# Kernel tuning notes

Measured on AMD Instinct MI355X. Metric: run time of the kernel, lower is better.

## Reference

```python
import jax, jax.numpy as jnp
import numpy as np

N_NODES = 100000
N_EDGES = 600000
D = 128


def gcn_conv(x, W, b, src, dst, n_nodes):
    """PyG-style GCNConv: add self-loops, symmetric deg^{-1/2} normalization."""
    xw = x @ W  # [N, out]
    # degree of destination nodes, counting the added self-loop
    deg = jnp.zeros((n_nodes,), xw.dtype).at[dst].add(1.0) + 1.0
    dinv = jax.lax.rsqrt(deg)
    coef = dinv[src] * dinv[dst]  # [E]
    agg = jnp.zeros_like(xw).at[dst].add(xw[src] * coef[:, None])
    agg = agg + xw * (dinv * dinv)[:, None]  # self-loop term
    return agg + b


def setup_inputs() -> dict:
    key = jax.random.key(0)
    k = jax.random.split(key, 9)
    s = 1.0 / np.sqrt(D)
    return {
        "x": jax.random.normal(k[0], (N_NODES, D), jnp.float32),
        "edge_index_pos": jax.random.randint(k[1], (2, N_EDGES), 0, N_NODES, jnp.int64),
        "edge_index_neg": jax.random.randint(k[2], (2, N_EDGES), 0, N_NODES, jnp.int64),
        "W1": jax.random.uniform(k[3], (D, D), jnp.float32, -s, s),
        "b1": jnp.zeros((D,), jnp.float32),
        "W2": jax.random.uniform(k[4], (D, D), jnp.float32, -s, s),
        "b2": jnp.zeros((D,), jnp.float32),
        "weight": jax.random.uniform(k[5], (2 * D, D), jnp.float32, -s, s),
        "bias": jnp.zeros((D,), jnp.float32),
    }


def reference(x, edge_index_pos, edge_index_neg, W1, b1, W2, b2, weight, bias):
    n = x.shape[0]
    h1 = gcn_conv(x, W1, b1, edge_index_pos[0], edge_index_pos[1], n)  # [N, D]
    h2 = gcn_conv(x, W2, b2, edge_index_neg[0], edge_index_neg[1], n)  # [N, D]
    h = jnp.concatenate([h1, h2], axis=-1)  # [N, 2D]
    return h @ weight + bias  # [N, D]
```

## Files before the change

kernel.cpp:

```cpp
#include <hip/hip_runtime.h>

#define N_NODES 100000
#define NT (2 * N_NODES)
#define D 128
#define N_EDGES 600000
#define ET (2 * N_EDGES)
#define CAP 32
#define XBLK 12500
#define EGRID ((ET + 255) / 256)
#define FROWS 256
#define FBLK ((N_NODES + FROWS - 1) / FROWS)
#define NBLK2 ((NT + 255) / 256)

typedef __attribute__((ext_vector_type(8))) short bf16x8;
typedef __attribute__((ext_vector_type(4))) float f32x4;

__device__ __forceinline__ unsigned short f2bf(float f) {
    union { float f; unsigned u; } v; v.f = f;
    unsigned r = (v.u + 0x7fff + ((v.u >> 16) & 1)) >> 16;
    return (unsigned short)r;
}
__device__ __forceinline__ float bf2f(unsigned short h) {
    union { unsigned u; float f; } v; v.u = ((unsigned)h) << 16;
    return v.f;
}

__device__ __forceinline__ long long load_idx(const void* e, long long i, int is32) {
    if (is32) return (long long)((const int*)e)[i];
    return ((const long long*)e)[i];
}

__device__ __forceinline__ int self_detect(const unsigned long long* __restrict__ e) {
    unsigned long long v = e[threadIdx.x & 63];
    unsigned long long m = __ballot(v > 0xFFFFFFFFull);
    return (m != 0ull) ? 1 : 0;
}

__global__ void prep_x2bf_degree(const float* __restrict__ W1, const float* __restrict__ W2,
                                 const float* __restrict__ weight,
                                 const float* __restrict__ b1, const float* __restrict__ b2,
                                 const float* __restrict__ bias,
                                 const float* __restrict__ x, unsigned short* __restrict__ xb,
                                 const void* __restrict__ ep, const void* __restrict__ en,
                                 unsigned short* __restrict__ Mt, float* __restrict__ bt,
                                 int* __restrict__ cnt) {
    const int b = blockIdx.x;
    if (b < 128) {
        int idx = b * 256 + threadIdx.x;
        int j = idx >> 8, k = idx & 255;
        float a = 0.f;
        if (k < D) {
            for (int d = 0; d < D; ++d) a += W1[k * D + d] * weight[d * D + j];
        } else {
            for (int d = 0; d < D; ++d) a += W2[(k - D) * D + d] * weight[(D + d) * D + j];
        }
        Mt[j * 256 + k] = f2bf(a);
    } else if (b == 128) {
        int t = threadIdx.x;
        if (t < D) {
            float a = bias[t];
            for (int k = 0; k < D; ++k)
                a += b1[k] * weight[k * D + t] + b2[k] * weight[(D + k) * D + t];
            bt[t] = a;
        }
    } else if (b < 129 + XBLK) {
        long long t = (long long)(b - 129) * 256 + threadIdx.x;
        float4 a = ((const float4*)x)[t];
        ((ushort4*)xb)[t] = make_ushort4(f2bf(a.x), f2bf(a.y), f2bf(a.z), f2bf(a.w));
    } else {
        int is32 = self_detect((const unsigned long long*)ep);
        int i = (b - 129 - XBLK) * 256 + threadIdx.x;
        if (i >= ET) return;
        int conv = (i >= N_EDGES);
        const void* e = conv ? en : ep;
        int j = conv ? i - N_EDGES : i;
        long long d = load_idx(e, (long long)N_EDGES + j, is32);
        atomicAdd(&cnt[conv * N_NODES + (int)d], 1);
    }
}

__global__ void make_dinv(const int* __restrict__ cnt, float* __restrict__ dinv,
                          unsigned char* __restrict__ degb) {
    int i = blockIdx.x * 256 + threadIdx.x;
    if (i < NT) {
        int v = cnt[i];
        dinv[i] = rsqrtf((float)v + 1.0f);
        degb[i] = (unsigned char)(v > 255 ? 255 : v);
    }
}

__global__ void ell_fill(const void* __restrict__ ep_, const void* __restrict__ en_,
                         const unsigned char* __restrict__ degb,
                         int* __restrict__ cnt, unsigned* __restrict__ ell) {
    int is32 = self_detect((const unsigned long long*)ep_);
    int i = blockIdx.x * blockDim.x + threadIdx.x;
    if (i >= ET) return;
    int conv = (i >= N_EDGES);
    const void* e = conv ? en_ : ep_;
    int j = conv ? i - N_EDGES : i;
    int si = (int)load_idx(e, j, is32);
    int di = (int)load_idx(e, (long long)N_EDGES + j, is32);
    int g = conv * N_NODES;
    int node = g + di;
    int slot = atomicSub(&cnt[node], 1) - 1;
    if (slot >= 0 && slot < CAP) {
        unsigned degS = degb[g + si];
        ell[(size_t)node * CAP + slot] = (unsigned)si | (degS << 20);
    }
}

__global__ __launch_bounds__(1024) void fused_gather_gemm(
    const unsigned char* __restrict__ degb, const unsigned* __restrict__ ell,
    const unsigned short* __restrict__ xb, const float* __restrict__ dinv,
    const unsigned short* __restrict__ Mt, const float* __restrict__ bt,
    float* __restrict__ out) {
    __shared__ unsigned short mlds[128][264];
    int t = threadIdx.x;
    for (int c = t; c < 4096; c += 1024) {
        int row = c >> 5;
        int kc = (c & 31) * 8;
        *(ulonglong2*)&mlds[row][kc] = *(const ulonglong2*)&Mt[row * 256 + kc];
    }
    __syncthreads();

    int wave = t >> 6, lane = t & 63;
    int rl = lane & 15, q = lane >> 4;
    int gr = blockIdx.x * FROWS + wave * 16 + rl;
    const bool valid = gr < N_NODES;

    bf16x8 af[8];
    #pragma unroll
    for (int conv = 0; conv < 2; ++conv) {
        float acc[4][8];
        if (valid) {
            int n = conv * N_NODES + gr;
            float dn = dinv[n];
            float f = dn * dn;
            const unsigned short* xr = xb + (size_t)gr * D + q * 8;
            #pragma unroll
            for (int m = 0; m < 4; ++m) {
                bf16x8 v = *(const bf16x8*)(xr + m * 32);
                #pragma unroll
                for (int j = 0; j < 8; ++j) acc[m][j] = bf2f((unsigned short)v[j]) * f;
            }
            int deg = degb[n];
            if (deg > CAP) deg = CAP;
            const unsigned* ep = ell + (size_t)n * CAP;
            int e = 0;
            for (; e + 1 < deg; e += 2) {
                unsigned c0 = ep[e], c1 = ep[e + 1];
                const unsigned short* p0 = xb + (size_t)(c0 & 0xFFFFF) * D + q * 8;
                const unsigned short* p1 = xb + (size_t)(c1 & 0xFFFFF) * D + q * 8;
                bf16x8 a0 = *(const bf16x8*)(p0);
                bf16x8 a1 = *(const bf16x8*)(p0 + 32);
                bf16x8 a2 = *(const bf16x8*)(p0 + 64);
                bf16x8 a3 = *(const bf16x8*)(p0 + 96);
                bf16x8 b0 = *(const bf16x8*)(p1);
                bf16x8 b1 = *(const bf16x8*)(p1 + 32);
                bf16x8 b2 = *(const bf16x8*)(p1 + 64);
                bf16x8 b3 = *(const bf16x8*)(p1 + 96);
                float coef0 = dn * rsqrtf((float)(c0 >> 20) + 1.0f);
                float coef1 = dn * rsqrtf((float)(c1 >> 20) + 1.0f);
                #pragma unroll
                for (int j = 0; j < 8; ++j) {
                    acc[0][j] += coef0 * bf2f((unsigned short)a0[j]);
                    acc[1][j] += coef0 * bf2f((unsigned short)a1[j]);
                    acc[2][j] += coef0 * bf2f((unsigned short)a2[j]);
                    acc[3][j] += coef0 * bf2f((unsigned short)a3[j]);
                }
                #pragma unroll
                for (int j = 0; j < 8; ++j) {
                    acc[0][j] += coef1 * bf2f((unsigned short)b0[j]);
                    acc[1][j] += coef1 * bf2f((unsigned short)b1[j]);
                    acc[2][j] += coef1 * bf2f((unsigned short)b2[j]);
                    acc[3][j] += coef1 * bf2f((unsigned short)b3[j]);
                }
            }
            if (e < deg) {
                unsigned c0 = ep[e];
                const unsigned short* p0 = xb + (size_t)(c0 & 0xFFFFF) * D + q * 8;
                bf16x8 a0 = *(const bf16x8*)(p0);
                bf16x8 a1 = *(const bf16x8*)(p0 + 32);
                bf16x8 a2 = *(const bf16x8*)(p0 + 64);
                bf16x8 a3 = *(const bf16x8*)(p0 + 96);
                float coef0 = dn * rsqrtf((float)(c0 >> 20) + 1.0f);
                #pragma unroll
                for (int j = 0; j < 8; ++j) {
                    acc[0][j] += coef0 * bf2f((unsigned short)a0[j]);
                    acc[1][j] += coef0 * bf2f((unsigned short)a1[j]);
                    acc[2][j] += coef0 * bf2f((unsigned short)a2[j]);
                    acc[3][j] += coef0 * bf2f((unsigned short)a3[j]);
                }
            }
        } else {
            #pragma unroll
            for (int m = 0; m < 4; ++m)
                #pragma unroll
                for (int j = 0; j < 8; ++j) acc[m][j] = 0.f;
        }
        #pragma unroll
        for (int m = 0; m < 4; ++m) {
            bf16x8 a;
            #pragma unroll
            for (int j = 0; j < 8; ++j) a[j] = (short)f2bf(acc[m][j]);
            af[conv * 4 + m] = a;
        }
    }

    f32x4 C[8];
    #pragma unroll
    for (int i = 0; i < 8; ++i) C[i] = (f32x4){0.f, 0.f, 0.f, 0.f};
    #pragma unroll
    for (int ks = 0; ks < 8; ++ks) {
        bf16x8 afr = af[ks];
        #pragma unroll
        for (int ct = 0; ct < 8; ++ct) {
            bf16x8 bfr = *(const bf16x8*)&mlds[ct * 16 + rl][ks * 32 + q * 8];
            C[ct] = __builtin_amdgcn_mfma_f32_16x16x32_bf16(afr, bfr, C[ct], 0, 0, 0);
        }
    }

    int orow = blockIdx.x * FROWS + wave * 16 + q * 4;
    #pragma unroll
    for (int ct = 0; ct < 8; ++ct) {
        int col = ct * 16 + rl;
        float b = bt[col];
        #pragma unroll
        for (int reg = 0; reg < 4; ++reg) {
            int row = orow + reg;
            if (row < N_NODES) out[(long long)row * D + col] = C[ct][reg] + b;
        }
    }
}

extern "C" void kernel_launch(void* const* d_in, const int* in_sizes, int n_in,
                              void* d_out, int out_size, void* d_ws, size_t ws_size,
                              hipStream_t stream) {
    const float* x      = (const float*)d_in[0];
    const void*  e_pos  = d_in[1];
    const void*  e_neg  = d_in[2];
    const float* W1     = (const float*)d_in[3];
    const float* b1     = (const float*)d_in[4];
    const float* W2     = (const float*)d_in[5];
    const float* b2     = (const float*)d_in[6];
    const float* weight = (const float*)d_in[7];
    const float* bias   = (const float*)d_in[8];
    float* out = (float*)d_out;

    unsigned short* xb = (unsigned short*)d_ws;
    unsigned short* Mt = xb + (size_t)N_NODES * D;
    float* bt   = (float*)(Mt + 128 * 256);
    float* dinv = bt + D;
    int*   cnt  = (int*)(dinv + NT);
    unsigned char* degb = (unsigned char*)(cnt + NT);
    unsigned* ell = (unsigned*)(degb + NT);

    hipMemsetAsync(cnt, 0, NT * sizeof(int), stream);
    prep_x2bf_degree<<<129 + XBLK + EGRID, 256, 0, stream>>>(
        W1, W2, weight, b1, b2, bias, x, xb, e_pos, e_neg, Mt, bt, cnt);
    make_dinv<<<NBLK2, 256, 0, stream>>>(cnt, dinv, degb);
    ell_fill<<<EGRID, 256, 0, stream>>>(e_pos, e_neg, degb, cnt, ell);
    fused_gather_gemm<<<FBLK, 1024, 0, stream>>>(degb, ell, xb, dinv, Mt, bt, out);
}
```

Before: 237.3 us.

## Sort nodes by degree pair to balance gather work within waves

Builds a 2D histogram of the clamped (pos, neg) in-degrees, prefix-scans it in every block and writes a node permutation ordered by degree key. The fused gather/GEMM kernel processes nodes in that permuted order and scatters its output rows back to their original positions. The intent is to cut lane divergence in the ELL gather loop, since the 16 rows of an MFMA tile then have similar degrees. The costs are an extra atomic histogram pass, a redundant per-block scan, an indirect perm load, and output writes that are no longer contiguous.

After: 356.5 us. 50.2% more time.

```diff
diff --git a/kernel.cpp b/kernel.cpp
--- a/kernel.cpp
+++ b/kernel.cpp
@@ -11,6 +11,8 @@
 #define FROWS 256
 #define FBLK ((N_NODES + FROWS - 1) / FROWS)
 #define NBLK2 ((NT + 255) / 256)
+#define NKEY 1089
+#define PBLK ((N_NODES + 255) / 256)
 
 typedef __attribute__((ext_vector_type(8))) short bf16x8;
 typedef __attribute__((ext_vector_type(4))) float f32x4;
@@ -80,36 +82,82 @@
 }
 
 __global__ void make_dinv(const int* __restrict__ cnt, float* __restrict__ dinv,
-                          unsigned char* __restrict__ degb) {
+                          unsigned char* __restrict__ degb, int* __restrict__ hist) {
     int i = blockIdx.x * 256 + threadIdx.x;
     if (i < NT) {
         int v = cnt[i];
         dinv[i] = rsqrtf((float)v + 1.0f);
         degb[i] = (unsigned char)(v > 255 ? 255 : v);
-    }
-}
-
-__global__ void ell_fill(const void* __restrict__ ep_, const void* __restrict__ en_,
+        if (i < N_NODES) {
+            int d2 = cnt[N_NODES + i];
+            int k1 = v > 32 ? 32 : v;
+            int k2 = d2 > 32 ? 32 : d2;
+            atomicAdd(&hist[k1 * 33 + k2], 1);
+        }
+    }
+}
+
+__global__ void perm_ell(const void* __restrict__ ep_, const void* __restrict__ en_,
                          const unsigned char* __restrict__ degb,
-                         int* __restrict__ cnt, unsigned* __restrict__ ell) {
-    int is32 = self_detect((const unsigned long long*)ep_);
-    int i = blockIdx.x * blockDim.x + threadIdx.x;
-    if (i >= ET) return;
-    int conv = (i >= N_EDGES);
-    const void* e = conv ? en_ : ep_;
-    int j = conv ? i - N_EDGES : i;
-    int si = (int)load_idx(e, j, is32);
-    int di = (int)load_idx(e, (long long)N_EDGES + j, is32);
-    int g = conv * N_NODES;
-    int node = g + di;
-    int slot = atomicSub(&cnt[node], 1) - 1;
-    if (slot >= 0 && slot < CAP) {
-        unsigned degS = degb[g + si];
-        ell[(size_t)node * CAP + slot] = (unsigned)si | (degS << 20);
+                         const int* __restrict__ hist, int* __restrict__ cur,
+                         int* __restrict__ cnt, int* __restrict__ perm,
+                         unsigned* __restrict__ ell) {
+    const int b = blockIdx.x;
+    if (b < PBLK) {
+        __shared__ int hb[NKEY];
+        __shared__ int bs[256];
+        int t = threadIdx.x;
+        for (int c = t; c < NKEY; c += 256) hb[c] = hist[c];
+        __syncthreads();
+        int k0 = t * 5;
+        int s = 0;
+        #pragma unroll
+        for (int u = 0; u < 5; ++u) { int k = k0 + u; if (k < NKEY) s += hb[k]; }
+        bs[t] = s;
+        __syncthreads();
+        int v = s;
+        for (int ofs = 1; ofs < 256; ofs <<= 1) {
+            int add = (t >= ofs) ? bs[t - ofs] : 0;
+            __syncthreads();
+            bs[t] += add;
+            __syncthreads();
+        }
+        int run = bs[t] - v;
+        #pragma unroll
+        for (int u = 0; u < 5; ++u) {
+            int k = k0 + u;
+            if (k < NKEY) { int h = hb[k]; hb[k] = run; run += h; }
+        }
+        __syncthreads();
+        int n = b * 256 + t;
+        if (n < N_NODES) {
+            int d1 = degb[n];            if (d1 > 32) d1 = 32;
+            int d2 = degb[N_NODES + n];  if (d2 > 32) d2 = 32;
+            int key = d1 * 33 + d2;
+            int slot = hb[key] + atomicAdd(&cur[key], 1);
+            perm[N_NODES - 1 - slot] = n;
+        }
+    } else {
+        int is32 = self_detect((const unsigned long long*)ep_);
+        int i = (b - PBLK) * 256 + threadIdx.x;
+        if (i >= ET) return;
+        int conv = (i >= N_EDGES);
+        const void* e = conv ? en_ : ep_;
+        int j = conv ? i - N_EDGES : i;
+        int si = (int)load_idx(e, j, is32);
+        int di = (int)load_idx(e, (long long)N_EDGES + j, is32);
+        int g = conv * N_NODES;
+        int node = g + di;
+        int slot = atomicSub(&cnt[node], 1) - 1;
+        if (slot >= 0 && slot < CAP) {
+            unsigned degS = degb[g + si];
+            ell[(size_t)node * CAP + slot] = (unsigned)si | (degS << 20);
+        }
     }
 }
 
 __global__ __launch_bounds__(1024) void fused_gather_gemm(
+    const int* __restrict__ perm,
     const unsigned char* __restrict__ degb, const unsigned* __restrict__ ell,
     const unsigned short* __restrict__ xb, const float* __restrict__ dinv,
     const unsigned short* __restrict__ Mt, const float* __restrict__ bt,
@@ -125,8 +173,9 @@
 
     int wave = t >> 6, lane = t & 63;
     int rl = lane & 15, q = lane >> 4;
-    int gr = blockIdx.x * FROWS + wave * 16 + rl;
-    const bool valid = gr < N_NODES;
+    int gidx = blockIdx.x * FROWS + wave * 16 + rl;
+    const bool valid = gidx < N_NODES;
+    int gr = valid ? perm[gidx] : 0;
 
     bf16x8 af[8];
     #pragma unroll
@@ -220,15 +269,20 @@
         }
     }
 
-    int orow = blockIdx.x * FROWS + wave * 16 + q * 4;
+    int gbase = blockIdx.x * FROWS + wave * 16 + q * 4;
+    int rowp[4];
+    #pragma unroll
+    for (int reg = 0; reg < 4; ++reg) {
+        int gi = gbase + reg;
+        rowp[reg] = (gi < N_NODES) ? perm[gi] : -1;
+    }
     #pragma unroll
     for (int ct = 0; ct < 8; ++ct) {
         int col = ct * 16 + rl;
         float b = bt[col];
         #pragma unroll
         for (int reg = 0; reg < 4; ++reg) {
-            int row = orow + reg;
-            if (row < N_NODES) out[(long long)row * D + col] = C[ct][reg] + b;
+            if (rowp[reg] >= 0) out[(long long)rowp[reg] * D + col] = C[ct][reg] + b;
         }
     }
 }
@@ -252,13 +306,16 @@
     float* bt   = (float*)(Mt + 128 * 256);
     float* dinv = bt + D;
     int*   cnt  = (int*)(dinv + NT);
-    unsigned char* degb = (unsigned char*)(cnt + NT);
+    int*   hist = cnt + NT;
+    int*   cur  = hist + NKEY;
+    int*   perm = cur + NKEY;
+    unsigned char* degb = (unsigned char*)(perm + N_NODES);
     unsigned* ell = (unsigned*)(degb + NT);
 
-    hipMemsetAsync(cnt, 0, NT * sizeof(int), stream);
+    hipMemsetAsync(cnt, 0, (NT + 2 * NKEY) * sizeof(int), stream);
     prep_x2bf_degree<<<129 + XBLK + EGRID, 256, 0, stream>>>(
         W1, W2, weight, b1, b2, bias, x, xb, e_pos, e_neg, Mt, bt, cnt);
-    make_dinv<<<NBLK2, 256, 0, stream>>>(cnt, dinv, degb);
-    ell_fill<<<EGRID, 256, 0, stream>>>(e_pos, e_neg, degb, cnt, ell);
-    fused_gather_gemm<<<FBLK, 1024, 0, stream>>>(degb, ell, xb, dinv, Mt, bt, out);
-}
+    make_dinv<<<NBLK2, 256, 0, stream>>>(cnt, dinv, degb, hist);
+    perm_ell<<<PBLK + EGRID, 256, 0, stream>>>(e_pos, e_neg, degb, hist, cur, cnt, perm, ell);
+    fused_gather_gemm<<<FBLK, 1024, 0, stream>>>(perm, degb, ell, xb, dinv, Mt, bt, out);
+}
```
